# Optimization experiments

Hardware: AMD Instinct MI355X
Metric: run time of the kernel (lower is better)

Reference implementation:

```python
import jax, jax.numpy as jnp
import numpy as np

N, D_IN, H, D_EMB = 2048, 128, 256, 64


def setup_inputs() -> dict:
    key = jax.random.key(0)
    ks = jax.random.split(key, 8)
    x = jax.random.normal(ks[0], (N, D_IN), dtype=jnp.float32)
    adj = jnp.zeros((N, N), dtype=jnp.float32)  # only its last dim is used (eye sizing)
    s = 0.05
    W0 = jax.random.normal(ks[1], (D_IN, H), dtype=jnp.float32) * s
    b0 = jnp.zeros((H,), dtype=jnp.float32)
    W1 = jax.random.normal(ks[2], (H, D_EMB), dtype=jnp.float32) * s
    b1 = jnp.zeros((D_EMB,), dtype=jnp.float32)
    W2 = jax.random.normal(ks[3], (D_IN, D_IN), dtype=jnp.float32) * s
    b2 = jnp.zeros((D_IN,), dtype=jnp.float32)
    temp = jnp.float32(0.1)
    theta = jnp.float32(0.1)
    return {"x": x, "adj": adj, "W0": W0, "b0": b0, "W1": W1, "b1": b1,
            "W2": W2, "b2": b2, "temp": temp, "theta": theta}


def reference(x, adj, W0, b0, W1, b1, W2, b2, temp, theta):
    # layer 0 (on x) and middle layer 1 (on out_x), both with ReLU activation
    out_x = jax.nn.relu(x @ W0 + b0)            # [N, H]
    emb = jax.nn.relu(out_x @ W1 + b1)          # [N, D_EMB]
    # last layer is applied to the ORIGINAL x (per the `x = model(x)` branch)
    x_last = x @ W2 + b2                        # [N, D_IN]

    # dist[i,j] = -||emb_i - emb_j||^2, computed via the gemm expansion
    sq = jnp.sum(emb * emb, axis=1)             # [N]
    dist = -(sq[:, None] + sq[None, :] - 2.0 * (emb @ emb.T))  # [N, N]

    prob = jax.nn.sigmoid((1.0 + temp) * dist + (5.0 + theta))
    A = prob + jnp.eye(adj.shape[-1], dtype=prob.dtype)        # [N, N]

    # diag(A.sum(-1))^{-1} @ A @ x_last  ==  rowwise divide by degree
    deg = jnp.sum(A, axis=-1)                   # [N]
    out = jax.nn.relu((A @ x_last) / deg[:, None])

    # sigmoid(.) > 0 everywhere, so all N*N entries are nonzero: adj_wts is the
    # full flattened adjacency (data-independent shape, jit-safe)
    adj_wts = A.reshape(-1)
    return out, adj_wts
```

## Files before the change

kernel.cpp:

```cpp
#include <hip/hip_runtime.h>
#include <hip/hip_bf16.h>


typedef short bf16x8 __attribute__((ext_vector_type(8)));
typedef float f32x4 __attribute__((ext_vector_type(4)));

__device__ __forceinline__ unsigned short f2bf(float f) {
    unsigned u = __float_as_uint(f);
    unsigned r = u + 0x7fffu + ((u >> 16) & 1u);
    return (unsigned short)(r >> 16);
}

__device__ __forceinline__ unsigned short f2bf_hu(float f) {
    return (unsigned short)((__float_as_uint(f) + 0x8000u) >> 16);
}

__device__ __forceinline__ bf16x8 pack_rne8(const float* p) {
    union { unsigned u[4]; bf16x8 v; } r;
    #pragma unroll
    for (int i = 0; i < 4; ++i) {
        unsigned lo = __float_as_uint(p[2 * i]) + 0x8000u;
        unsigned hi = __float_as_uint(p[2 * i + 1]) + 0x8000u;
        r.u[i] = __builtin_amdgcn_perm(hi, lo, 0x07060302u);
    }
    return r.v;
}

__device__ __forceinline__ bf16x8 pack_bf8(const float* p) {
    union { unsigned u[4]; bf16x8 v; } r;
    #pragma unroll
    for (int i = 0; i < 4; ++i)
        r.u[i] = __builtin_amdgcn_perm(__float_as_uint(p[2 * i + 1]),
                                       __float_as_uint(p[2 * i]), 0x07060302u);
    return r.v;
}

__global__ __launch_bounds__(256) void k0_prep(
    const float* __restrict__ W0, const float* __restrict__ W1,
    const float* __restrict__ W2,
    unsigned short* __restrict__ W0T,
    unsigned short* __restrict__ W1T,
    unsigned short* __restrict__ W2T)
{
    const int gid = blockIdx.x * 256 + threadIdx.x;
    {
        const int h = gid >> 7, k = gid & 127;
        W0T[gid] = f2bf_hu(W0[(size_t)k * 256 + h]);
    }
    if (gid < 16384) {
        const int h = gid >> 8, k = gid & 255;
        W1T[gid] = f2bf_hu(W1[(size_t)k * 64 + h]);
    } else {
        const int o = gid - 16384;
        const int c = o >> 7, k = o & 127;
        W2T[o] = f2bf_hu(W2[(size_t)k * 128 + c]);
    }
}

template<int VEC>
__global__ __launch_bounds__(256, 2) void k1_mfma(
    const float* __restrict__ x,
    const float* __restrict__ W0, const float* __restrict__ b0,
    const float* __restrict__ W1, const float* __restrict__ b1,
    const float* __restrict__ W2, const float* __restrict__ b2,
    const unsigned short* __restrict__ W0T,
    const unsigned short* __restrict__ W1T,
    const unsigned short* __restrict__ W2T,
    unsigned short* __restrict__ emb_bf,
    unsigned short* __restrict__ xlT_bf,
    float* __restrict__ sq)
{
    constexpr int LDO = 264;
    __shared__ unsigned short oxb[16 * LDO];
    __shared__ float sqs[4][16];

    const int t = threadIdx.x;
    const int lane = t & 63;
    const int w = t >> 6;
    const int m = lane & 15;
    const int q = lane >> 4;
    const int tile = blockIdx.x >> 1;
    const int role = blockIdx.x & 1;
    const int i0 = tile * 16;

    bf16x8 ax[4];
    #pragma unroll
    for (int kb = 0; kb < 4; ++kb) {
        float xf[8];
        *(f32x4*)&xf[0] = *(const f32x4*)(x + (size_t)(i0 + m) * 128 + kb * 32 + q * 8);
        *(f32x4*)&xf[4] = *(const f32x4*)(x + (size_t)(i0 + m) * 128 + kb * 32 + q * 8 + 4);
        ax[kb] = pack_rne8(xf);
    }

    if (role == 0) {
        const int h1 = w * 16 + m;
        const float bias1 = b1[h1];
        bf16x8 wp[8];
        #pragma unroll
        for (int kb = 0; kb < 8; ++kb) {
            if (VEC) {
                wp[kb] = *(const bf16x8*)(W1T + (size_t)h1 * 256 + kb * 32 + q * 8);
            } else {
                float wf[8];
                #pragma unroll
                for (int j = 0; j < 8; ++j) wf[j] = W1[(size_t)(kb * 32 + q * 8 + j) * 64 + h1];
                wp[kb] = pack_rne8(wf);
            }
        }

        #pragma unroll
        for (int hh = 0; hh < 4; ++hh) {
            const int h = (w * 4 + hh) * 16 + m;
            float bb = b0[h];
            f32x4 acc = {bb, bb, bb, bb};
            #pragma unroll
            for (int kb = 0; kb < 4; ++kb) {
                bf16x8 bfrag;
                if (VEC) {
                    bfrag = *(const bf16x8*)(W0T + (size_t)h * 128 + kb * 32 + q * 8);
                } else {
                    float wf[8];
                    #pragma unroll
                    for (int j = 0; j < 8; ++j) wf[j] = W0[(size_t)(kb * 32 + q * 8 + j) * 256 + h];
                    bfrag = pack_rne8(wf);
                }
                acc = __builtin_amdgcn_mfma_f32_16x16x32_bf16(ax[kb], bfrag, acc, 0, 0, 0);
            }
            #pragma unroll
            for (int r = 0; r < 4; ++r)
                oxb[(q * 4 + r) * LDO + h] = f2bf(fmaxf(acc[r], 0.0f));
        }
        __syncthreads();

        f32x4 acc = {bias1, bias1, bias1, bias1};
        #pragma unroll
        for (int kb = 0; kb < 8; ++kb) {
            bf16x8 af = *(const bf16x8*)(&oxb[m * LDO + kb * 32 + q * 8]);
            acc = __builtin_amdgcn_mfma_f32_16x16x32_bf16(af, wp[kb], acc, 0, 0, 0);
        }
        float s2[4];
        #pragma unroll
        for (int r = 0; r < 4; ++r) {
            float e = fmaxf(acc[r], 0.0f);
            emb_bf[(size_t)(i0 + q * 4 + r) * 64 + h1] = f2bf(e);
            s2[r] = e * e;
        }
        #pragma unroll
        for (int r = 0; r < 4; ++r) {
            float v = s2[r];
            v += __shfl_xor(v, 1);
            v += __shfl_xor(v, 2);
            v += __shfl_xor(v, 4);
            v += __shfl_xor(v, 8);
            if (m == 0) sqs[w][q * 4 + r] = v;
        }
        __syncthreads();
        if (t < 16)
            sq[i0 + t] = sqs[0][t] + sqs[1][t] + sqs[2][t] + sqs[3][t];
    } else {
        bf16x8 wp[8];
        #pragma unroll
        for (int hh = 0; hh < 2; ++hh) {
            const int c = (w * 2 + hh) * 16 + m;
            #pragma unroll
            for (int kb = 0; kb < 4; ++kb) {
                if (VEC) {
                    wp[hh * 4 + kb] = *(const bf16x8*)(W2T + (size_t)c * 128 + kb * 32 + q * 8);
                } else {
                    float wf[8];
                    #pragma unroll
                    for (int j = 0; j < 8; ++j) wf[j] = W2[(size_t)(kb * 32 + q * 8 + j) * 128 + c];
                    wp[hh * 4 + kb] = pack_rne8(wf);
                }
            }
        }
        #pragma unroll
        for (int hh = 0; hh < 2; ++hh) {
            const int c = (w * 2 + hh) * 16 + m;
            float bb = b2[c];
            f32x4 acc = {bb, bb, bb, bb};
            #pragma unroll
            for (int kb = 0; kb < 4; ++kb)
                acc = __builtin_amdgcn_mfma_f32_16x16x32_bf16(ax[kb], wp[hh * 4 + kb], acc, 0, 0, 0);
            uint2 pk;
            pk.x = (unsigned)f2bf(acc[0]) | ((unsigned)f2bf(acc[1]) << 16);
            pk.y = (unsigned)f2bf(acc[2]) | ((unsigned)f2bf(acc[3]) << 16);
            *(uint2*)(&xlT_bf[(size_t)c * 2048 + i0 + q * 4]) = pk;
        }
    }
}

__global__ __launch_bounds__(256, 2) void k2f(
    const unsigned short* __restrict__ emb_bf,
    const unsigned short* __restrict__ xlT_bf,
    const float* __restrict__ sq,
    const float* __restrict__ tempp, const float* __restrict__ thetap,
    float* __restrict__ adjw,
    float* __restrict__ outPart,
    float* __restrict__ degPart)
{
    constexpr int LDP = 132;
    __shared__ float Pt[2][16 * LDP];
    __shared__ float degS[4][16];

    const int t = threadIdx.x;
    const int lane = t & 63;
    const int w = t >> 6;
    const int m = lane & 15;
    const int q = lane >> 4;
    const int i0 = blockIdx.x * 16;
    const int bj = blockIdx.y;
    const int jstrip0 = bj * 256;
    const float scale = 1.0f + tempp[0];
    const float bias = 5.0f + thetap[0];

    bf16x8 a0 = *(const bf16x8*)(emb_bf + (size_t)(i0 + m) * 64 + q * 8);
    bf16x8 a1 = *(const bf16x8*)(emb_bf + (size_t)(i0 + m) * 64 + 32 + q * 8);
    float sqIr[4];
    #pragma unroll
    for (int r = 0; r < 4; ++r) sqIr[r] = sq[i0 + q * 4 + r];

    f32x4 accO0 = {0.f, 0.f, 0.f, 0.f};
    f32x4 accO1 = {0.f, 0.f, 0.f, 0.f};
    float dega[4] = {0.f, 0.f, 0.f, 0.f};
    const int cg = w * 32;

    #pragma unroll
    for (int jt = 0; jt < 2; ++jt) {
        const int j0 = jstrip0 + jt * 128;
        float* P = &Pt[jt][0];

        bf16x8 xb[8];
        #pragma unroll
        for (int s = 0; s < 4; ++s) {
            const int k = j0 + s * 32 + q * 8;
            xb[2 * s]     = *(const bf16x8*)(xlT_bf + (size_t)(cg + m) * 2048 + k);
            xb[2 * s + 1] = *(const bf16x8*)(xlT_bf + (size_t)(cg + 16 + m) * 2048 + k);
        }

        #pragma unroll
        for (int s = 0; s < 2; ++s) {
            const int col = (w * 2 + s) * 16 + m;
            const unsigned short* ebj = emb_bf + (size_t)(j0 + col) * 64;
            bf16x8 b0 = *(const bf16x8*)(ebj + q * 8);
            bf16x8 b1 = *(const bf16x8*)(ebj + 32 + q * 8);
            f32x4 S = {0.f, 0.f, 0.f, 0.f};
            S = __builtin_amdgcn_mfma_f32_16x16x32_bf16(a0, b0, S, 0, 0, 0);
            S = __builtin_amdgcn_mfma_f32_16x16x32_bf16(a1, b1, S, 0, 0, 0);

            const float csqJ = sq[j0 + col];
            const int gcol = j0 + col;
            #pragma unroll
            for (int r = 0; r < 4; ++r) {
                int grow = i0 + q * 4 + r;
                float dist = 2.0f * S[r] - sqIr[r] - csqJ;
                float z = scale * dist + bias;
                float p = __builtin_amdgcn_rcpf(1.0f + __expf(-z));
                if (grow == gcol) p += 1.0f;
                dega[r] += p;
                P[(q * 4 + r) * LDP + col] = p;
            }
        }
        __syncthreads();

        {
            int row = t >> 5;
            int c0 = (t & 31) * 4;
            f32x4 v0 = *(const f32x4*)(&P[row * LDP + c0]);
            f32x4 v1 = *(const f32x4*)(&P[(row + 8) * LDP + c0]);
            *(f32x4*)(adjw + (size_t)(i0 + row) * 2048 + j0 + c0) = v0;
            *(f32x4*)(adjw + (size_t)(i0 + row + 8) * 2048 + j0 + c0) = v1;
        }

        #pragma unroll
        for (int s = 0; s < 4; ++s) {
            float af[8];
            *(f32x4*)(&af[0]) = *(const f32x4*)(&P[m * LDP + s * 32 + q * 8]);
            *(f32x4*)(&af[4]) = *(const f32x4*)(&P[m * LDP + s * 32 + q * 8 + 4]);
            bf16x8 aa = pack_bf8(af);
            accO0 = __builtin_amdgcn_mfma_f32_16x16x32_bf16(aa, xb[2 * s], accO0, 0, 0, 0);
            accO1 = __builtin_amdgcn_mfma_f32_16x16x32_bf16(aa, xb[2 * s + 1], accO1, 0, 0, 0);
        }
    }

    #pragma unroll
    for (int r = 0; r < 4; ++r) {
        float v = dega[r];
        v += __shfl_xor(v, 1);
        v += __shfl_xor(v, 2);
        v += __shfl_xor(v, 4);
        v += __shfl_xor(v, 8);
        if (m == 0) degS[w][q * 4 + r] = v;
    }
    __syncthreads();
    if (t < 16)
        degPart[bj * 2048 + i0 + t] =
            degS[0][t] + degS[1][t] + degS[2][t] + degS[3][t];

    float2* opf2 = (float2*)outPart + ((size_t)bj * 128 + blockIdx.x) * 1024;
    #pragma unroll
    for (int r = 0; r < 4; ++r) {
        float2 pk;
        pk.x = accO0[r];
        pk.y = accO1[r];
        opf2[((q * 4 + r) * 4 + w) * 16 + m] = pk;
    }
}

__global__ __launch_bounds__(256) void k3_fin(
    const float* __restrict__ outPart, const float* __restrict__ degPart,
    float* __restrict__ out)
{
    int gid = blockIdx.x * 256 + threadIdx.x;
    int i = gid >> 6;
    int wm = gid & 63;
    int w = wm >> 4, m = wm & 15;
    int tile = i >> 4, rit = i & 15;
    size_t base = (size_t)tile * 2048 + (size_t)((rit * 4 + w) * 16 + m) * 2;
    float s0 = 0.f, s1 = 0.f, d = 0.f;
    #pragma unroll
    for (int p = 0; p < 8; ++p) {
        const float* src = outPart + (size_t)p * 262144 + base;
        s0 += src[0];
        s1 += src[1];
        d += degPart[p * 2048 + i];
    }
    float dinv = 1.0f / d;
    out[(size_t)i * 128 + w * 32 + m] = fmaxf(s0 * dinv, 0.f);
    out[(size_t)i * 128 + w * 32 + 16 + m] = fmaxf(s1 * dinv, 0.f);
}

extern "C" void kernel_launch(void* const* d_in, const int* in_sizes, int n_in,
                              void* d_out, int out_size, void* d_ws, size_t ws_size,
                              hipStream_t stream) {
    (void)in_sizes; (void)n_in; (void)out_size;
    const float* x     = (const float*)d_in[0];
    const float* W0    = (const float*)d_in[2];
    const float* b0    = (const float*)d_in[3];
    const float* W1    = (const float*)d_in[4];
    const float* b1    = (const float*)d_in[5];
    const float* W2    = (const float*)d_in[6];
    const float* b2    = (const float*)d_in[7];
    const float* temp  = (const float*)d_in[8];
    const float* theta = (const float*)d_in[9];

    char* ws = (char*)d_ws;
    unsigned short* emb_bf = (unsigned short*)(ws);
    unsigned short* xlT_bf = (unsigned short*)(ws + 262144);
    float* sq      = (float*)(ws + 786432);
    float* degPart = (float*)(ws + 794624);
    float* outPart = (float*)(ws + 860160);
    unsigned short* W0T = (unsigned short*)(ws + 9248768);
    unsigned short* W1T = (unsigned short*)(ws + 9314304);
    unsigned short* W2T = (unsigned short*)(ws + 9347072);
    const bool vec = (ws_size >= 9379840);

    float* out  = (float*)d_out;
    float* adjw = (float*)d_out + 262144;

    if (vec) {
        k0_prep<<<128, 256, 0, stream>>>(W0, W1, W2, W0T, W1T, W2T);
        k1_mfma<1><<<256, 256, 0, stream>>>(x, W0, b0, W1, b1, W2, b2,
                                            W0T, W1T, W2T, emb_bf, xlT_bf, sq);
    } else {
        k1_mfma<0><<<256, 256, 0, stream>>>(x, W0, b0, W1, b1, W2, b2,
                                            W0T, W1T, W2T, emb_bf, xlT_bf, sq);
    }
    k2f<<<dim3(128, 8), 256, 0, stream>>>(emb_bf, xlT_bf, sq, temp, theta,
                                          adjw, outPart, degPart);
    k3_fin<<<512, 256, 0, stream>>>(outPart, degPart, out);
}
```

Baseline: 108.9 us.

## Split pairwise kernel into more column strips with nontemporal adjacency stores

Templates the pairwise kernel on the number of 128-column tiles per block. When the workspace is large enough it launches 16 strips of one tile each instead of 8 strips of two, doubling the grid and raising the occupancy hint to 8 blocks per CU. The 16 MB adjacency output is now written with nontemporal stores to avoid polluting the cache. In exchange, the finalize kernel must reduce twice as many partial outputs, and a larger workspace is required.

```diff
diff --git a/kernel.cpp b/kernel.cpp
--- a/kernel.cpp
+++ b/kernel.cpp
@@ -190,7 +190,8 @@
     }
 }
 
-__global__ __launch_bounds__(256, 2) void k2f(
+template<int JT>
+__global__ __launch_bounds__(256, 8) void k2f(
     const unsigned short* __restrict__ emb_bf,
     const unsigned short* __restrict__ xlT_bf,
     const float* __restrict__ sq,
@@ -200,7 +201,7 @@
     float* __restrict__ degPart)
 {
     constexpr int LDP = 132;
-    __shared__ float Pt[2][16 * LDP];
+    __shared__ float Pt[JT][16 * LDP];
     __shared__ float degS[4][16];
 
     const int t = threadIdx.x;
@@ -210,7 +211,6 @@
     const int q = lane >> 4;
     const int i0 = blockIdx.x * 16;
     const int bj = blockIdx.y;
-    const int jstrip0 = bj * 256;
     const float scale = 1.0f + tempp[0];
     const float bias = 5.0f + thetap[0];
 
@@ -226,8 +226,8 @@
     const int cg = w * 32;
 
     #pragma unroll
-    for (int jt = 0; jt < 2; ++jt) {
-        const int j0 = jstrip0 + jt * 128;
+    for (int jt = 0; jt < JT; ++jt) {
+        const int j0 = (bj * JT + jt) * 128;
         float* P = &Pt[jt][0];
 
         bf16x8 xb[8];
@@ -268,8 +268,8 @@
             int c0 = (t & 31) * 4;
             f32x4 v0 = *(const f32x4*)(&P[row * LDP + c0]);
             f32x4 v1 = *(const f32x4*)(&P[(row + 8) * LDP + c0]);
-            *(f32x4*)(adjw + (size_t)(i0 + row) * 2048 + j0 + c0) = v0;
-            *(f32x4*)(adjw + (size_t)(i0 + row + 8) * 2048 + j0 + c0) = v1;
+            __builtin_nontemporal_store(v0, (f32x4*)(adjw + (size_t)(i0 + row) * 2048 + j0 + c0));
+            __builtin_nontemporal_store(v1, (f32x4*)(adjw + (size_t)(i0 + row + 8) * 2048 + j0 + c0));
         }
 
         #pragma unroll
@@ -281,6 +281,7 @@
             accO0 = __builtin_amdgcn_mfma_f32_16x16x32_bf16(aa, xb[2 * s], accO0, 0, 0, 0);
             accO1 = __builtin_amdgcn_mfma_f32_16x16x32_bf16(aa, xb[2 * s + 1], accO1, 0, 0, 0);
         }
+        if (JT > 1 && jt + 1 < JT) __syncthreads();
     }
 
     #pragma unroll
@@ -307,6 +308,7 @@
     }
 }
 
+template<int NP>
 __global__ __launch_bounds__(256) void k3_fin(
     const float* __restrict__ outPart, const float* __restrict__ degPart,
     float* __restrict__ out)
@@ -319,7 +321,7 @@
     size_t base = (size_t)tile * 2048 + (size_t)((rit * 4 + w) * 16 + m) * 2;
     float s0 = 0.f, s1 = 0.f, d = 0.f;
     #pragma unroll
-    for (int p = 0; p < 8; ++p) {
+    for (int p = 0; p < NP; ++p) {
         const float* src = outPart + (size_t)p * 262144 + base;
         s0 += src[0];
         s1 += src[1];
@@ -345,28 +347,39 @@
     const float* theta = (const float*)d_in[9];
 
     char* ws = (char*)d_ws;
-    unsigned short* emb_bf = (unsigned short*)(ws);
-    unsigned short* xlT_bf = (unsigned short*)(ws + 262144);
-    float* sq      = (float*)(ws + 786432);
-    float* degPart = (float*)(ws + 794624);
-    float* outPart = (float*)(ws + 860160);
-    unsigned short* W0T = (unsigned short*)(ws + 9248768);
-    unsigned short* W1T = (unsigned short*)(ws + 9314304);
-    unsigned short* W2T = (unsigned short*)(ws + 9347072);
-    const bool vec = (ws_size >= 9379840);
-
     float* out  = (float*)d_out;
     float* adjw = (float*)d_out + 262144;
 
-    if (vec) {
+    const bool big = (ws_size >= 17833984);
+
+    if (big) {
+        unsigned short* emb_bf = (unsigned short*)(ws);
+        unsigned short* xlT_bf = (unsigned short*)(ws + 262144);
+        float* sq      = (float*)(ws + 786432);
+        float* degPart = (float*)(ws + 794624);
+        float* outPart = (float*)(ws + 925696);
+        unsigned short* W0T = (unsigned short*)(ws + 17702912);
+        unsigned short* W1T = (unsigned short*)(ws + 17768448);
+        unsigned short* W2T = (unsigned short*)(ws + 17801216);
+
         k0_prep<<<128, 256, 0, stream>>>(W0, W1, W2, W0T, W1T, W2T);
         k1_mfma<1><<<256, 256, 0, stream>>>(x, W0, b0, W1, b1, W2, b2,
                                             W0T, W1T, W2T, emb_bf, xlT_bf, sq);
+        k2f<1><<<dim3(128, 16), 256, 0, stream>>>(emb_bf, xlT_bf, sq, temp, theta,
+                                                  adjw, outPart, degPart);
+        k3_fin<16><<<512, 256, 0, stream>>>(outPart, degPart, out);
     } else {
+        unsigned short* emb_bf = (unsigned short*)(ws);
+        unsigned short* xlT_bf = (unsigned short*)(ws + 262144);
+        float* sq      = (float*)(ws + 786432);
+        float* degPart = (float*)(ws + 794624);
+        float* outPart = (float*)(ws + 860160);
+
         k1_mfma<0><<<256, 256, 0, stream>>>(x, W0, b0, W1, b1, W2, b2,
-                                            W0T, W1T, W2T, emb_bf, xlT_bf, sq);
-    }
-    k2f<<<dim3(128, 8), 256, 0, stream>>>(emb_bf, xlT_bf, sq, temp, theta,
-                                          adjw, outPart, degPart);
-    k3_fin<<<512, 256, 0, stream>>>(outPart, degPart, out);
-}
+                                            nullptr, nullptr, nullptr,
+                                            emb_bf, xlT_bf, sq);
+        k2f<2><<<dim3(128, 8), 256, 0, stream>>>(emb_bf, xlT_bf, sq, temp, theta,
+                                                 adjw, outPart, degPart);
+        k3_fin<8><<<512, 256, 0, stream>>>(outPart, degPart, out);
+    }
+}
```

Measured after the change: 128.9 us. +18.3%, slower.
